# Optimization experiments

Hardware: AMD Instinct MI355X
Metric: run time of the kernel (lower is better)

The kernel has to match this reference:

```python
import jax, jax.numpy as jnp
import numpy as np

B, T, W, D = 2, 64, 32, 512
H = 8                      # n_heads
N = 64                     # d_state
EXPAND = 2
DIN = EXPAND * D           # 1024 d_inner
R = -(-D // 16)            # dt_rank = ceil(d_model/16) = 32
K = 4                      # d_conv (mamba default)


def setup_inputs():
    key = jax.random.key(0)
    ks = jax.random.split(key, 20)
    s = 0.02
    inp = {
        'x': jax.random.normal(ks[0], (B, T, W, D), jnp.float32),
        'wq': jax.random.normal(ks[1], (D, D), jnp.float32) * s,
        'bq': jnp.zeros((D,), jnp.float32),
        'wk': jax.random.normal(ks[2], (D, D), jnp.float32) * s,
        'bk': jnp.zeros((D,), jnp.float32),
        'wv': jax.random.normal(ks[3], (D, D), jnp.float32) * s,
        'bv': jnp.zeros((D,), jnp.float32),
        'wo': jax.random.normal(ks[4], (D, D), jnp.float32) * s,
        'bo': jnp.zeros((D,), jnp.float32),
        'in_proj_w': jax.random.normal(ks[5], (2 * DIN, D), jnp.float32) * s,
        'conv_w': jax.random.normal(ks[6], (DIN, 1, K), jnp.float32) * 0.2,
        'conv_b': jnp.zeros((DIN,), jnp.float32),
        'x_proj_w': jax.random.normal(ks[7], (R + 2 * N, DIN), jnp.float32) * s,
        'dt_proj_w': jax.random.normal(ks[8], (DIN, R), jnp.float32) * 0.1,
        'dt_proj_b': jnp.full((DIN,), -4.6, jnp.float32),  # ~softplus^-1(0.01)
        'A_log': jnp.log(jnp.broadcast_to(jnp.arange(1, N + 1, dtype=jnp.float32), (DIN, N))),
        'D_param': jnp.ones((DIN,), jnp.float32),
        'out_proj_w': jax.random.normal(ks[9], (D, DIN), jnp.float32) * s,
        'ln_w': jnp.ones((D,), jnp.float32),
        'ln_b': jnp.zeros((D,), jnp.float32),
    }
    return inp


def _attention(xf, wq, bq, wk, bk, wv, bv, wo, bo):
    b, L, d = xf.shape
    e = d // H
    q = (xf @ wq.T + bq).reshape(b, L, H, e)
    k = (xf @ wk.T + bk).reshape(b, L, H, e)
    v = (xf @ wv.T + bv).reshape(b, L, H, e)
    scale = 1.0 / jnp.sqrt(jnp.float32(e))
    scores = jnp.einsum('blhe,bshe->bhls', q, k) * scale
    causal = jnp.tril(jnp.ones((L, L), bool))
    scores = jnp.where(causal, scores, jnp.finfo(scores.dtype).min)
    attn = jax.nn.softmax(scores, axis=-1)  # dropout off (eval mode)
    out = jnp.einsum('bhls,bshe->blhe', attn, v).reshape(b, L, d)
    return out @ wo.T + bo


def _mamba(xf, in_proj_w, conv_w, conv_b, x_proj_w, dt_proj_w, dt_proj_b,
           A_log, D_param, out_proj_w):
    b, L, d = xf.shape
    xz = xf @ in_proj_w.T                 # (B,L,2*DIN)
    x_in, z = jnp.split(xz, 2, axis=-1)
    # causal depthwise conv1d over L
    xc = jnp.transpose(x_in, (0, 2, 1))   # (B,DIN,L)
    xc = jax.lax.conv_general_dilated(
        xc, conv_w, window_strides=(1,), padding=[(K - 1, 0)],
        feature_group_count=DIN, dimension_numbers=('NCH', 'OIH', 'NCH'))
    xc = xc + conv_b[None, :, None]
    u = jax.nn.silu(jnp.transpose(xc, (0, 2, 1)))   # (B,L,DIN)
    dbc = u @ x_proj_w.T                             # (B,L,R+2N)
    dt, Bm, Cm = dbc[..., :R], dbc[..., R:R + N], dbc[..., R + N:]
    dt = jax.nn.softplus(dt @ dt_proj_w.T + dt_proj_b)  # (B,L,DIN)
    A = -jnp.exp(A_log)                                 # (DIN,N)

    def step(h, t):
        dt_t, B_t, C_t, u_t = t  # (b,DIN),(b,N),(b,N),(b,DIN)
        dA = jnp.exp(dt_t[..., None] * A)                       # (b,DIN,N)
        h = dA * h + (dt_t * u_t)[..., None] * B_t[:, None, :]  # (b,DIN,N)
        y = jnp.einsum('bdn,bn->bd', h, C_t)
        return h, y

    h0 = jnp.zeros((b, DIN, N), xf.dtype)
    xs = (jnp.swapaxes(dt, 0, 1), jnp.swapaxes(Bm, 0, 1),
          jnp.swapaxes(Cm, 0, 1), jnp.swapaxes(u, 0, 1))
    _, ys = jax.lax.scan(step, h0, xs)
    y = jnp.swapaxes(ys, 0, 1) + u * D_param   # (B,L,DIN)
    y = y * jax.nn.silu(z)
    return y @ out_proj_w.T


def reference(x, wq, bq, wk, bk, wv, bv, wo, bo, in_proj_w, conv_w, conv_b,
              x_proj_w, dt_proj_w, dt_proj_b, A_log, D_param, out_proj_w,
              ln_w, ln_b):
    b, t, w, d = x.shape
    L = t * w
    xf = x.reshape(b, L, d)
    x_attn = _attention(xf, wq, bq, wk, bk, wv, bv, wo, bo).reshape(b, t, w, d)
    x_mamba = _mamba(xf, in_proj_w, conv_w, conv_b, x_proj_w, dt_proj_w,
                     dt_proj_b, A_log, D_param, out_proj_w).reshape(b, t, w, d)
    h = x + x_attn + x_mamba
    mu = jnp.mean(h, axis=-1, keepdims=True)
    var = jnp.mean(jnp.square(h - mu), axis=-1, keepdims=True)
    return (h - mu) * jax.lax.rsqrt(var + 1e-5) * ln_w + ln_b
```

## Files before the change

kernel.cpp:

```cpp
#include <hip/hip_runtime.h>

typedef __attribute__((ext_vector_type(4))) float f32x4;
typedef __attribute__((ext_vector_type(8))) short short8;
typedef __attribute__((ext_vector_type(2))) unsigned uint2e;

#define DEV static __device__ __forceinline__

DEV ushort f2b(float f) {
  union { float f; unsigned u; } v; v.f = f;
  unsigned r = v.u + 0x7FFF + ((v.u >> 16) & 1);
  return (ushort)(r >> 16);
}
DEV unsigned pack_bf2(float lo, float hi) {
  return (unsigned)f2b(lo) | ((unsigned)f2b(hi) << 16);
}
DEV float bflo(unsigned p) { return __uint_as_float(p << 16); }
DEV float bfhi(unsigned p) { return __uint_as_float(p & 0xFFFF0000u); }
DEV float b2f(ushort u) { return __uint_as_float((unsigned)u << 16); }

DEV float fexp2(float x) { float r; asm("v_exp_f32 %0, %1" : "=v"(r) : "v"(x)); return r; }

DEV float xor32_add_lo(float s) {
  uint2e r = __builtin_amdgcn_permlane32_swap(__float_as_uint(s), __float_as_uint(s), false, false);
  return s + __uint_as_float(r.x);
}

#define QP(x, ctrl) __int_as_float(__builtin_amdgcn_update_dpp(0, __float_as_int(x), (ctrl), 0xf, 0xf, false))
#define SWZ(x, off) __int_as_float(__builtin_amdgcn_ds_swizzle(__float_as_int(x), (off)))
#define DPP_ADD(x, ctrl, rmask) \
  ((x) + __int_as_float(__builtin_amdgcn_update_dpp(0, __float_as_int(x), (ctrl), (rmask), 0xf, false)))

#define LOG2E 1.44269504f

#define BB    2
#define LL    2048
#define DD    512
#define HH    8
#define EE    64
#define DIN   1024
#define NS    64
#define RR    32
#define BL    4096
#define NCH   16
#define TC    128
#define NC    1536
#define MFMA(a,b,c) __builtin_amdgcn_mfma_f32_16x16x32_bf16((a),(b),(c),0,0,0)

struct CvtJobs {
  const float* src[7];
  ushort*      dst[7];
  int          n[7];
};

__global__ __launch_bounds__(256) void cvt_multi(CvtJobs j) {
  int job = blockIdx.y;
  const float* s = j.src[job];
  ushort* d = j.dst[job];
  int n = j.n[job];
  for (int i = blockIdx.x * 256 + threadIdx.x; i < n; i += gridDim.x * 256)
    d[i] = f2b(s[i]);
}

__global__ __launch_bounds__(256) void pack_wcomb(
    const float* __restrict__ wo, const float* __restrict__ opw,
    const float* __restrict__ bq, const float* __restrict__ bk,
    const float* __restrict__ bv, ushort* __restrict__ wc,
    float* __restrict__ bqkv)
{
  int i = blockIdx.x * 256 + threadIdx.x;
  if (i < NC) bqkv[i] = (i < DD) ? bq[i] : ((i < 2 * DD) ? bk[i - DD] : bv[i - 2 * DD]);
  if (i >= DD * NC) return;
  int n = i / NC, c = i - n * NC;
  float v = (c < DD) ? wo[n * DD + c] : opw[n * DIN + (c - DD)];
  wc[i] = f2b(v);
}

__global__ __launch_bounds__(256) void gemm_bt(
    const ushort* __restrict__ A, const ushort* __restrict__ W,
    const float* __restrict__ bias, float* __restrict__ outF,
    ushort* __restrict__ outB, int M, int N, int K, int act)
{
  __shared__ ushort As[64][40];
  __shared__ ushort Ws[64][40];
  int m0 = blockIdx.y * 64, n0 = blockIdx.x * 64;
  int tid = threadIdx.x, l = tid & 63, w = tid >> 6;
  int wm = (w >> 1) * 32, wn = (w & 1) * 32;
  int lr = l & 15, kl = (l >> 4) * 8;
  int srow = tid >> 2, sk = (tid & 3) * 8;
  f32x4 acc[2][2] = {};

  for (int k0 = 0; k0 < K; k0 += 32) {
    uint4 av = *(const uint4*)&A[(size_t)(m0 + srow) * K + k0 + sk];
    uint4 wv;
    if (n0 + srow < N) wv = *(const uint4*)&W[(size_t)(n0 + srow) * K + k0 + sk];
    else { wv.x = 0; wv.y = 0; wv.z = 0; wv.w = 0; }
    *(uint4*)&As[srow][sk] = av;
    *(uint4*)&Ws[srow][sk] = wv;
    __syncthreads();
    short8 a0 = *(const short8*)&As[wm + lr][kl];
    short8 a1 = *(const short8*)&As[wm + 16 + lr][kl];
    short8 b0 = *(const short8*)&Ws[wn + lr][kl];
    short8 b1 = *(const short8*)&Ws[wn + 16 + lr][kl];
    acc[0][0] = MFMA(a0, b0, acc[0][0]);
    acc[0][1] = MFMA(a0, b1, acc[0][1]);
    acc[1][0] = MFMA(a1, b0, acc[1][0]);
    acc[1][1] = MFMA(a1, b1, acc[1][1]);
    __syncthreads();
  }

  #pragma unroll
  for (int mi = 0; mi < 2; mi++)
    #pragma unroll
    for (int ni = 0; ni < 2; ni++) {
      int rbase = m0 + wm + mi * 16 + ((l >> 4) << 2);
      int col = n0 + wn + ni * 16 + lr;
      if (col < N) {
        float bval = bias ? bias[col] : 0.f;
        #pragma unroll
        for (int r = 0; r < 4; r++) {
          float v = acc[mi][ni][r] + bval;
          if (act == 1) v = (v > 20.f) ? v : log1pf(__expf(v));
          size_t o = (size_t)(rbase + r) * N + col;
          if (outF) outF[o] = v;
          if (outB) outB[o] = f2b(v);
        }
      }
    }
}

__global__ __launch_bounds__(256) void gemm128(
    const ushort* __restrict__ A, const ushort* __restrict__ W,
    const float* __restrict__ bias, float* __restrict__ outF,
    ushort* __restrict__ outB, int M, int N, int K)
{
  __shared__ ushort As[128][40];
  __shared__ ushort Ws[128][40];
  int tid = threadIdx.x, l = tid & 63, w = tid >> 6;
  int m0 = blockIdx.y * 128, n0 = blockIdx.x * 128;
  int wm = (w >> 1) * 64, wn = (w & 1) * 64;
  int lr = l & 15, kl = (l >> 4) * 8;
  int srow = tid >> 1, sk = (tid & 1) * 16;
  f32x4 acc[4][4] = {};

  const ushort* Ap = A + (size_t)(m0 + srow) * K + sk;
  const ushort* Wp = W + (size_t)(n0 + srow) * K + sk;

  for (int k0 = 0; k0 < K; k0 += 32) {
    uint4 a0 = *(const uint4*)(Ap);
    uint4 a1 = *(const uint4*)(Ap + 8);
    uint4 b0 = *(const uint4*)(Wp);
    uint4 b1 = *(const uint4*)(Wp + 8);
    __syncthreads();
    *(uint4*)&As[srow][sk]     = a0;
    *(uint4*)&As[srow][sk + 8] = a1;
    *(uint4*)&Ws[srow][sk]     = b0;
    *(uint4*)&Ws[srow][sk + 8] = b1;
    __syncthreads();
    short8 af[4], bf[4];
    #pragma unroll
    for (int mi = 0; mi < 4; mi++) af[mi] = *(const short8*)&As[wm + mi * 16 + lr][kl];
    #pragma unroll
    for (int ni = 0; ni < 4; ni++) bf[ni] = *(const short8*)&Ws[wn + ni * 16 + lr][kl];
    #pragma unroll
    for (int mi = 0; mi < 4; mi++)
      #pragma unroll
      for (int ni = 0; ni < 4; ni++)
        acc[mi][ni] = MFMA(af[mi], bf[ni], acc[mi][ni]);
    Ap += 32; Wp += 32;
  }

  #pragma unroll
  for (int mi = 0; mi < 4; mi++)
    #pragma unroll
    for (int ni = 0; ni < 4; ni++) {
      int rbase = m0 + wm + mi * 16 + ((l >> 4) << 2);
      int col = n0 + wn + ni * 16 + lr;
      float bval = bias ? bias[col] : 0.f;
      #pragma unroll
      for (int r = 0; r < 4; r++) {
        float v = acc[mi][ni][r] + bval;
        size_t o = (size_t)(rbase + r) * N + col;
        if (outF) outF[o] = v;
        if (outB) outB[o] = f2b(v);
      }
    }
}

__global__ __launch_bounds__(256) void flash_attn(
    const ushort* __restrict__ qkv, ushort* __restrict__ comb)
{
  __shared__ ushort Qs[64][72];
  __shared__ ushort Ks[64][72];
  __shared__ ushort Vt[64][72];
  __shared__ ushort Ps[64][72];

  int qt = 31 - blockIdx.x;
  int h = blockIdx.y, b = blockIdx.z;
  int tid = threadIdx.x, l = tid & 63, w = tid >> 6;
  int w16 = w * 16, lr = l & 15, kl = (l >> 4) * 8;

  for (int i = tid; i < 512; i += 256) {
    int row = i >> 3, c8 = (i & 7) * 8;
    *(uint4*)&Qs[row][c8] =
        *(const uint4*)&qkv[((size_t)(b * LL + qt * 64 + row)) * NC + h * EE + c8];
  }
  __syncthreads();

  float m_r[4] = {-1e30f, -1e30f, -1e30f, -1e30f};
  float l_r[4] = {0.f, 0.f, 0.f, 0.f};
  f32x4 oacc[4] = {};
  const float SSC = 0.125f * LOG2E;

  for (int kv = 0; kv <= qt; kv++) {
    for (int i = tid; i < 512; i += 256) {
      int s = i >> 3, c8 = (i & 7) * 8;
      size_t rb = ((size_t)(b * LL + kv * 64 + s)) * NC + h * EE + c8;
      *(uint4*)&Ks[s][c8] = *(const uint4*)&qkv[rb + DD];
      uint4 vv = *(const uint4*)&qkv[rb + 2 * DD];
      const ushort* pv = (const ushort*)&vv;
      #pragma unroll
      for (int jj = 0; jj < 8; jj++) Vt[c8 + jj][s] = pv[jj];
    }
    __syncthreads();

    f32x4 sacc[4] = {};
    #pragma unroll
    for (int kk = 0; kk < 2; kk++) {
      short8 aq = *(const short8*)&Qs[w16 + lr][kk * 32 + kl];
      #pragma unroll
      for (int nt = 0; nt < 4; nt++) {
        short8 bk8 = *(const short8*)&Ks[nt * 16 + lr][kk * 32 + kl];
        sacc[nt] = MFMA(aq, bk8, sacc[nt]);
      }
    }

    bool diag = (kv == qt);
    float scl[4];
    #pragma unroll
    for (int r = 0; r < 4; r++) {
      int rloc = w16 + ((l >> 4) << 2) + r;
      float sv[4];
      #pragma unroll
      for (int nt = 0; nt < 4; nt++) {
        float v = sacc[nt][r] * SSC;
        if (diag && (nt * 16 + lr) > rloc) v = -1e30f;
        sv[nt] = v;
      }
      float mx = fmaxf(fmaxf(sv[0], sv[1]), fmaxf(sv[2], sv[3]));
      mx = fmaxf(mx, QP(mx, 0xB1));
      mx = fmaxf(mx, QP(mx, 0x4E));
      mx = fmaxf(mx, SWZ(mx, 0x101F));
      mx = fmaxf(mx, SWZ(mx, 0x201F));
      float mnew = fmaxf(m_r[r], mx);
      float sc = fexp2(m_r[r] - mnew);
      float rs = 0.f;
      #pragma unroll
      for (int nt = 0; nt < 4; nt++) {
        float p = fexp2(sv[nt] - mnew);
        rs += p;
        Ps[rloc][nt * 16 + lr] = f2b(p);
      }
      rs += QP(rs, 0xB1);
      rs += QP(rs, 0x4E);
      rs += SWZ(rs, 0x101F);
      rs += SWZ(rs, 0x201F);
      l_r[r] = l_r[r] * sc + rs;
      m_r[r] = mnew;
      scl[r] = sc;
    }
    #pragma unroll
    for (int nt = 0; nt < 4; nt++)
      #pragma unroll
      for (int r = 0; r < 4; r++) oacc[nt][r] *= scl[r];

    #pragma unroll
    for (int kk = 0; kk < 2; kk++) {
      short8 ap = *(const short8*)&Ps[w16 + lr][kk * 32 + kl];
      #pragma unroll
      for (int nt = 0; nt < 4; nt++) {
        short8 bv8 = *(const short8*)&Vt[nt * 16 + lr][kk * 32 + kl];
        oacc[nt] = MFMA(ap, bv8, oacc[nt]);
      }
    }
    __syncthreads();
  }

  #pragma unroll
  for (int nt = 0; nt < 4; nt++)
    #pragma unroll
    for (int r = 0; r < 4; r++) {
      int row = qt * 64 + w16 + ((l >> 4) << 2) + r;
      float v = oacc[nt][r] / l_r[r];
      comb[((size_t)(b * LL + row)) * NC + h * EE + nt * 16 + lr] = f2b(v);
    }
}

__global__ __launch_bounds__(256) void conv_silu(
    const ushort* __restrict__ xz, const float* __restrict__ cw,
    const float* __restrict__ cb, ushort* __restrict__ ub)
{
  int i = blockIdx.x * 256 + threadIdx.x;
  if (i >= BL * DIN) return;
  int d = i & (DIN - 1);
  int bl = i >> 10;
  int t = bl & (LL - 1);
  int b = bl >> 11;
  float s = cb[d];
  #pragma unroll
  for (int j = 0; j < 4; j++) {
    int tt = t - 3 + j;
    if (tt >= 0) s += b2f(xz[((size_t)(b * LL + tt)) * (2 * DIN) + d]) * cw[d * 4 + j];
  }
  float r = s / (1.f + __expf(-s));
  ub[i] = f2b(r);
}

__global__ __launch_bounds__(256) void slice_dt(
    const float* __restrict__ dbc, ushort* __restrict__ dtc)
{
  int i = blockIdx.x * 256 + threadIdx.x;
  if (i >= BL * RR) return;
  int m = i >> 5, r = i & 31;
  dtc[i] = f2b(dbc[m * 160 + r]);
}

__global__ __launch_bounds__(256) void pack_bc(
    const float* __restrict__ dbc, unsigned* __restrict__ bbp,
    float4* __restrict__ bcp4)
{
  int i = blockIdx.x * 256 + threadIdx.x;
  if (i >= BB * (LL / 2) * NS) return;
  int n = i & 63, tp = (i >> 6) & 1023, b = i >> 16;
  size_t r0 = ((size_t)(b * LL + 2 * tp)) * 160;
  float B0 = dbc[r0 + 32 + n],  C0 = dbc[r0 + 96 + n];
  float B1 = dbc[r0 + 192 + n], C1 = dbc[r0 + 256 + n];
  bbp[i] = pack_bf2(B0, B1);
  bcp4[i] = make_float4(B0, C0, B1, C1);
}

__global__ __launch_bounds__(256) void pack_dtu(
    const ushort* __restrict__ dtb16, const ushort* __restrict__ ub,
    const ushort* __restrict__ xz, const float* __restrict__ dpar,
    unsigned* __restrict__ dtu_p, unsigned* __restrict__ sg_p)
{
  __shared__ float s_dt[32][65], s_du[32][65], s_gz[32][65], s_ug[32][65];
  int d0 = blockIdx.x * 64, t0 = blockIdx.y * 32;
  int tid = threadIdx.x;
  int c = tid & 63, r4 = tid >> 6;
  float Dv = dpar[d0 + c];
  #pragma unroll
  for (int k = 0; k < 8; k++) {
    int r = k * 4 + r4;
    size_t row = (size_t)(t0 + r);
    float dtv = b2f(dtb16[row * DIN + d0 + c]);
    float uv  = b2f(ub   [row * DIN + d0 + c]);
    float zz  = b2f(xz   [row * (2 * DIN) + DIN + d0 + c]);
    float g = zz / (1.f + __expf(-zz));
    s_dt[r][c] = dtv;
    s_du[r][c] = dtv * uv;
    s_gz[r][c] = g;
    s_ug[r][c] = uv * Dv * g;
  }
  __syncthreads();
  int dl = tid >> 2, q = tid & 3;
  int b = t0 >> 11, tl0 = t0 & (LL - 1);
  size_t obase = ((size_t)(b * DIN + d0 + dl)) * LL + tl0 + q * 8;
  #pragma unroll
  for (int tt = 0; tt < 8; tt++) {
    int t = q * 8 + tt;
    dtu_p[obase + tt] = pack_bf2(s_dt[t][dl], s_du[t][dl]);
    sg_p [obase + tt] = pack_bf2(s_gz[t][dl], s_ug[t][dl]);
  }
}

__global__ __launch_bounds__(256) void scan_phase1(
    const unsigned* __restrict__ dtu_p, const unsigned* __restrict__ bbp,
    const float* __restrict__ alog, float* __restrict__ hf, float* __restrict__ ap)
{
  __shared__ float lds[4][TC][2];
  int tid = threadIdx.x, w = tid >> 6, l = tid & 63;
  int wid = blockIdx.x * 4 + w;
  int d = wid & (DIN - 1);
  int c = (wid >> 10) & (NCH - 1);
  int b = wid >> 14;
  float An2 = -__expf(alog[d * NS + l]) * LOG2E;

  size_t pbase = ((size_t)(b * DIN + d)) * LL + c * TC;
  unsigned p0 = dtu_p[pbase + l];
  unsigned p1 = dtu_p[pbase + 64 + l];
  float s0 = bflo(p0), s1 = bflo(p1);
  s0 = DPP_ADD(s0, 0x111, 0xf); s0 = DPP_ADD(s0, 0x112, 0xf);
  s0 = DPP_ADD(s0, 0x114, 0xf); s0 = DPP_ADD(s0, 0x118, 0xf);
  s0 = DPP_ADD(s0, 0x142, 0xa); s0 = DPP_ADD(s0, 0x143, 0xc);
  s1 = DPP_ADD(s1, 0x111, 0xf); s1 = DPP_ADD(s1, 0x112, 0xf);
  s1 = DPP_ADD(s1, 0x114, 0xf); s1 = DPP_ADD(s1, 0x118, 0xf);
  s1 = DPP_ADD(s1, 0x142, 0xa); s1 = DPP_ADD(s1, 0x143, 0xc);
  float T0 = __uint_as_float(__builtin_amdgcn_readlane(__float_as_uint(s0), 63));
  float T  = T0 + __uint_as_float(__builtin_amdgcn_readlane(__float_as_uint(s1), 63));
  lds[w][l][0]      = T - s0;
  lds[w][l][1]      = bfhi(p0);
  lds[w][64 + l][0] = (T - T0) - s1;
  lds[w][64 + l][1] = bfhi(p1);
  __syncthreads();

  const unsigned* bq = bbp + ((size_t)(b * 1024 + c * 64) * 64 + l);
  float h0 = 0.f, h1 = 0.f;
  for (int g = 0; g < 16; g++) {
    unsigned bv[4];
    #pragma unroll
    for (int k = 0; k < 4; k++) bv[k] = bq[k * 64];
    const float* gb = &lds[w][g * 8][0];
    #pragma unroll
    for (int j = 0; j < 8; j++) {
      float2 dd = *(const float2*)(gb + j * 2);
      float Bv = (j & 1) ? bfhi(bv[j >> 1]) : bflo(bv[j >> 1]);
      float a = fexp2(dd.x * An2);
      if (j & 1) h1 += a * (dd.y * Bv);
      else       h0 += a * (dd.y * Bv);
    }
    bq += 256;
  }
  size_t o = (((size_t)((b << 10) + d) * NCH) + c) * 64 + l;
  hf[o] = h0 + h1;
  ap[o] = fexp2(T * An2);
}

__global__ __launch_bounds__(256) void scan_carry(
    const float* __restrict__ hf, const float* __restrict__ ap,
    float* __restrict__ carry)
{
  int i = blockIdx.x * 256 + threadIdx.x;
  int n = i & 63;
  int d = (i >> 6) & (DIN - 1);
  int b = i >> 16;
  size_t base = ((size_t)((b << 10) + d) * NCH) * 64 + n;
  float cur = 0.f;
  #pragma unroll
  for (int c = 0; c < NCH; c++) {
    carry[base + (size_t)c * 64] = cur;
    cur = ap[base + (size_t)c * 64] * cur + hf[base + (size_t)c * 64];
  }
}

__global__ __launch_bounds__(256) void scan_phase3(
    const unsigned* __restrict__ dtu_p, const unsigned* __restrict__ sg_p,
    const float4* __restrict__ bcp4, const float* __restrict__ alog,
    const float* __restrict__ carry, ushort* __restrict__ ymt)
{
  __shared__ float lds[4][TC][4];
  __shared__ ushort yt[4][TC];
  int tid = threadIdx.x, w = tid >> 6, l = tid & 63;
  int wid = blockIdx.x * 4 + w;
  int d = wid & (DIN - 1);
  int c = (wid >> 10) & (NCH - 1);
  int b = wid >> 14;
  float An2 = -__expf(alog[d * NS + l]) * LOG2E;

  size_t pbase = ((size_t)(b * DIN + d)) * LL + c * TC;
  #pragma unroll
  for (int q = 0; q < 2; q++) {
    unsigned pd = dtu_p[pbase + q * 64 + l];
    unsigned pg = sg_p [pbase + q * 64 + l];
    lds[w][q * 64 + l][0] = bflo(pd);
    lds[w][q * 64 + l][1] = bfhi(pd);
    lds[w][q * 64 + l][2] = bflo(pg);
    lds[w][q * 64 + l][3] = bfhi(pg);
  }
  __syncthreads();

  float h = carry[(((size_t)((b << 10) + d) * NCH) + c) * 64 + l];
  const float4* bq = bcp4 + ((size_t)(b * 1024 + c * 64) * 64 + l);
  bool s1f = l & 1, s2f = l & 2, s4f = l & 4;
  bool wl = l < 8;

  for (int g = 0; g < 16; g++) {
    float4 bcs[4];
    bcs[0] = bq[0]; bcs[1] = bq[64]; bcs[2] = bq[128]; bcs[3] = bq[192];
    const float* gb = &lds[w][g * 8][0];
    float p[8];
    #pragma unroll
    for (int j = 0; j < 8; j++) {
      float2 dd = *(const float2*)(gb + j * 4);
      float Bv = (j & 1) ? bcs[j >> 1].z : bcs[j >> 1].x;
      float Cv = (j & 1) ? bcs[j >> 1].w : bcs[j >> 1].y;
      float a = fexp2(dd.x * An2);
      h = a * h + dd.y * Bv;
      p[j] = h * Cv;
    }
    #pragma unroll
    for (int j = 0; j < 8; j++) p[j] += QP(p[j], 0xB1);
    float q0 = s1f ? p[1] : p[0];
    float q1 = s1f ? p[3] : p[2];
    float q2 = s1f ? p[5] : p[4];
    float q3 = s1f ? p[7] : p[6];
    q0 += QP(q0, 0x4E); q1 += QP(q1, 0x4E);
    q2 += QP(q2, 0x4E); q3 += QP(q3, 0x4E);
    float r0 = s2f ? q1 : q0;
    float r1 = s2f ? q3 : q2;
    r0 += SWZ(r0, 0x101F); r1 += SWZ(r1, 0x101F);
    float s = s4f ? r1 : r0;
    s += QP(s, 0x128);
    s += SWZ(s, 0x401F);
    s = xor32_add_lo(s);

    float2 sgv = *(const float2*)(&lds[w][g * 8 + (l & 7)][2]);
    if (wl) yt[w][g * 8 + l] = f2b(s * sgv.x + sgv.y);
    bq += 256;
  }
  __syncthreads();
  unsigned vv = *(const unsigned*)&yt[w][2 * l];
  ((unsigned*)(ymt + pbase))[l] = vv;
}

__global__ __launch_bounds__(256) void transpose_ym(
    const ushort* __restrict__ ymt, ushort* __restrict__ comb)
{
  __shared__ ushort tile[64][72];
  int tid = threadIdx.x;
  int bx = blockIdx.x;
  int by = blockIdx.y;
  int b  = blockIdx.z;
  int r = tid >> 2, c16 = (tid & 3) * 16;
  const ushort* src = ymt + ((size_t)(b * DIN + bx * 64 + r)) * LL + by * 64 + c16;
  *(uint4*)&tile[r][c16]     = *(const uint4*)src;
  *(uint4*)&tile[r][c16 + 8] = *(const uint4*)(src + 8);
  __syncthreads();
  ushort tmp[16];
  #pragma unroll
  for (int j = 0; j < 16; j++) tmp[j] = tile[c16 + j][r];
  ushort* dst = comb + ((size_t)(b * LL + by * 64 + r)) * NC + DD + bx * 64 + c16;
  *(uint4*)dst       = *(uint4*)&tmp[0];
  *(uint4*)(dst + 8) = *(uint4*)&tmp[8];
}

__global__ __launch_bounds__(256) void residual_ln(
    const float* __restrict__ x, const float* __restrict__ so,
    const float* __restrict__ lw, const float* __restrict__ lb,
    float* __restrict__ out)
{
  int row = blockIdx.x * 4 + (threadIdx.x >> 6);
  int l = threadIdx.x & 63;
  size_t base = (size_t)row * DD;
  float h[8];
  float s = 0.f, s2 = 0.f;
  #pragma unroll
  for (int half = 0; half < 2; half++) {
    int c = half * 256 + l * 4;
    float4 xv = *(const float4*)(x + base + c);
    float4 sv = *(const float4*)(so + base + c);
    float* hp = h + half * 4;
    hp[0] = xv.x + sv.x;
    hp[1] = xv.y + sv.y;
    hp[2] = xv.z + sv.z;
    hp[3] = xv.w + sv.w;
    #pragma unroll
    for (int j = 0; j < 4; j++) { s += hp[j]; s2 += hp[j] * hp[j]; }
  }
  #pragma unroll
  for (int o = 1; o < 64; o <<= 1) { s += __shfl_xor(s, o); s2 += __shfl_xor(s2, o); }
  float mean = s * (1.f / DD);
  float var = s2 * (1.f / DD) - mean * mean;
  float rs = rsqrtf(var + 1e-5f);
  #pragma unroll
  for (int half = 0; half < 2; half++) {
    int c = half * 256 + l * 4;
    float4 ov;
    ov.x = (h[half*4+0] - mean) * rs * lw[c+0] + lb[c+0];
    ov.y = (h[half*4+1] - mean) * rs * lw[c+1] + lb[c+1];
    ov.z = (h[half*4+2] - mean) * rs * lw[c+2] + lb[c+2];
    ov.w = (h[half*4+3] - mean) * rs * lw[c+3] + lb[c+3];
    *(float4*)(out + base + c) = ov;
  }
}

extern "C" void kernel_launch(void* const* d_in, const int* in_sizes, int n_in,
                              void* d_out, int out_size, void* d_ws, size_t ws_size,
                              hipStream_t stream) {
  const float* x    = (const float*)d_in[0];
  const float* wq   = (const float*)d_in[1];
  const float* bq   = (const float*)d_in[2];
  const float* wk   = (const float*)d_in[3];
  const float* bk   = (const float*)d_in[4];
  const float* wv   = (const float*)d_in[5];
  const float* bv   = (const float*)d_in[6];
  const float* wo   = (const float*)d_in[7];
  const float* bo   = (const float*)d_in[8];
  const float* inw  = (const float*)d_in[9];
  const float* cw   = (const float*)d_in[10];
  const float* cb   = (const float*)d_in[11];
  const float* xpw  = (const float*)d_in[12];
  const float* dtw  = (const float*)d_in[13];
  const float* dtb  = (const float*)d_in[14];
  const float* alog = (const float*)d_in[15];
  const float* dpar = (const float*)d_in[16];
  const float* opw  = (const float*)d_in[17];
  const float* lnw  = (const float*)d_in[18];
  const float* lnb  = (const float*)d_in[19];

  char* ws = (char*)d_ws;
  size_t off = 0;
  auto alloc = [&](size_t bytes) -> void* {
    void* p = ws + off;
    off += (bytes + 255) & ~(size_t)255;
    return p;
  };

  const size_t BLD = (size_t)BL * DD;
  const size_t BLDIN = (size_t)BL * DIN;
  const size_t BLNC = (size_t)BL * NC;

  ushort* xf_b   = (ushort*)alloc(BLD * 2);
  ushort* wqkv_b = (ushort*)alloc((size_t)NC * DD * 2);
  float*  bqkv   = (float*)alloc(NC * 4);
  ushort* inw_b  = (ushort*)alloc(2 * DIN * DD * 2);
  ushort* xpw_b  = (ushort*)alloc(160 * DIN * 2);
  ushort* dtw_b  = (ushort*)alloc(DIN * RR * 2);
  ushort* wcomb_b= (ushort*)alloc((size_t)DD * NC * 2);
  ushort* qkv_b  = (ushort*)alloc(BLNC * 2);
  ushort* comb_a = (ushort*)alloc(BLNC * 2);
  float*  sum_o  = (float*)alloc(BLD * 4);
  ushort* xz_b   = (ushort*)alloc(BL * (size_t)(2 * DIN) * 2);
  ushort* u_b    = (ushort*)alloc(BLDIN * 2);
  float*  dbc    = (float*)alloc((size_t)BL * 160 * 4);
  ushort* dtc_b  = (ushort*)alloc((size_t)BL * RR * 2);
  ushort* dt_b   = (ushort*)alloc(BLDIN * 2);
  ushort* ymt_b  = (ushort*)alloc(BLDIN * 2);
  unsigned* bbp  = (unsigned*)alloc((size_t)BB * (LL / 2) * NS * 4);
  float4* bcp4   = (float4*)alloc((size_t)BB * (LL / 2) * NS * sizeof(float4));
  unsigned* dtu_p = (unsigned*)alloc(BLDIN * 4);
  unsigned* sg_p  = (unsigned*)alloc(BLDIN * 4);

  const size_t SCN = (size_t)BB * DIN * NCH * 64;
  float* hf_s    = (float*)xz_b;
  float* ap_s    = hf_s + SCN;
  float* carry_s = (float*)alloc(SCN * 4);

  CvtJobs cj;
  cj.src[0] = x;    cj.dst[0] = xf_b;                 cj.n[0] = (int)BLD;
  cj.src[1] = wq;   cj.dst[1] = wqkv_b;               cj.n[1] = DD * DD;
  cj.src[2] = wk;   cj.dst[2] = wqkv_b + DD * DD;     cj.n[2] = DD * DD;
  cj.src[3] = wv;   cj.dst[3] = wqkv_b + 2 * DD * DD; cj.n[3] = DD * DD;
  cj.src[4] = inw;  cj.dst[4] = inw_b;                cj.n[4] = 2 * DIN * DD;
  cj.src[5] = xpw;  cj.dst[5] = xpw_b;                cj.n[5] = 160 * DIN;
  cj.src[6] = dtw;  cj.dst[6] = dtw_b;                cj.n[6] = DIN * RR;
  cvt_multi<<<dim3(256, 7), 256, 0, stream>>>(cj);
  pack_wcomb<<<dim3((DD * NC + 255) / 256), 256, 0, stream>>>(wo, opw, bq, bk, bv, wcomb_b, bqkv);

  gemm128<<<dim3(12, 32), 256, 0, stream>>>(xf_b, wqkv_b, bqkv, nullptr, qkv_b, BL, NC, DD);

  flash_attn<<<dim3(32, HH, BB), 256, 0, stream>>>(qkv_b, comb_a);

  gemm128<<<dim3(16, 32), 256, 0, stream>>>(xf_b, inw_b, nullptr, nullptr, xz_b, BL, 2 * DIN, DD);

  conv_silu<<<dim3(32768), 256, 0, stream>>>(xz_b, cw, cb, u_b);

  gemm_bt<<<dim3(3, 64), 256, 0, stream>>>(u_b, xpw_b, nullptr, dbc, nullptr, BL, 160, DIN, 0);

  slice_dt<<<dim3(512), 256, 0, stream>>>(dbc, dtc_b);
  gemm_bt<<<dim3(16, 64), 256, 0, stream>>>(dtc_b, dtw_b, dtb, nullptr, dt_b, BL, DIN, RR, 1);

  pack_bc<<<dim3(512), 256, 0, stream>>>(dbc, bbp, bcp4);
  pack_dtu<<<dim3(16, 128), 256, 0, stream>>>(dt_b, u_b, xz_b, dpar, dtu_p, sg_p);
  scan_phase1<<<dim3(8192), 256, 0, stream>>>(dtu_p, bbp, alog, hf_s, ap_s);
  scan_carry<<<dim3(512), 256, 0, stream>>>(hf_s, ap_s, carry_s);
  scan_phase3<<<dim3(8192), 256, 0, stream>>>(dtu_p, sg_p, bcp4, alog, carry_s, ymt_b);
  transpose_ym<<<dim3(16, 32, BB), 256, 0, stream>>>(ymt_b, comb_a);

  gemm_bt<<<dim3(8, 64), 256, 0, stream>>>(comb_a, wcomb_b, bo, sum_o, nullptr, BL, DD, NC, 0);

  residual_ln<<<dim3(1024), 256, 0, stream>>>(x, sum_o, lnw, lnb, (float*)d_out);
}
```

Baseline: 398.5 us.

## Merge QKV and in_proj GEMMs and co-schedule attention with x_proj GEMM

Concatenates the QKV and Mamba in_proj weights into a single 3584-wide GEMM, so one launch produces q, k, v, x and z in a shared buffer. The flash attention kernel and the x_proj GEMM are then merged into one launch whose first 512 blocks do attention and whose remaining blocks do the small x_proj GEMM. The aim is to cut launch count and let the small GEMM fill idle CUs left by the causally imbalanced attention tail. The cost is a wider row stride for the attention and conv reads, and a simpler 64x64 x_proj tile path.

Result: faster. 380.1 us (-4.6%).

```diff
diff --git a/kernel.cpp b/kernel.cpp
--- a/kernel.cpp
+++ b/kernel.cpp
@@ -44,6 +44,9 @@
 #define NCH   16
 #define TC    128
 #define NC    1536
+#define NQ    3584
+#define XOFF  1536
+#define ZOFF  2560
 #define MFMA(a,b,c) __builtin_amdgcn_mfma_f32_16x16x32_bf16((a),(b),(c),0,0,0)
 
 struct CvtJobs {
@@ -65,10 +68,11 @@
     const float* __restrict__ wo, const float* __restrict__ opw,
     const float* __restrict__ bq, const float* __restrict__ bk,
     const float* __restrict__ bv, ushort* __restrict__ wc,
-    float* __restrict__ bqkv)
+    float* __restrict__ bqi)
 {
   int i = blockIdx.x * 256 + threadIdx.x;
-  if (i < NC) bqkv[i] = (i < DD) ? bq[i] : ((i < 2 * DD) ? bk[i - DD] : bv[i - 2 * DD]);
+  if (i < NQ)
+    bqi[i] = (i < DD) ? bq[i] : (i < 2 * DD) ? bk[i - DD] : (i < NC) ? bv[i - 2 * DD] : 0.f;
   if (i >= DD * NC) return;
   int n = i / NC, c = i - n * NC;
   float v = (c < DD) ? wo[n * DD + c] : opw[n * DIN + (c - DD)];
@@ -186,113 +190,161 @@
     }
 }
 
-__global__ __launch_bounds__(256) void flash_attn(
-    const ushort* __restrict__ qkv, ushort* __restrict__ comb)
-{
-  __shared__ ushort Qs[64][72];
-  __shared__ ushort Ks[64][72];
-  __shared__ ushort Vt[64][72];
-  __shared__ ushort Ps[64][72];
-
-  int qt = 31 - blockIdx.x;
-  int h = blockIdx.y, b = blockIdx.z;
+__global__ __launch_bounds__(256) void attn_xproj(
+    const ushort* __restrict__ qkv, ushort* __restrict__ comb,
+    const ushort* __restrict__ ub, const ushort* __restrict__ xpw,
+    float* __restrict__ dbc)
+{
+  __shared__ ushort smem[4 * 64 * 72];
+  int id = blockIdx.x;
   int tid = threadIdx.x, l = tid & 63, w = tid >> 6;
-  int w16 = w * 16, lr = l & 15, kl = (l >> 4) * 8;
-
-  for (int i = tid; i < 512; i += 256) {
-    int row = i >> 3, c8 = (i & 7) * 8;
-    *(uint4*)&Qs[row][c8] =
-        *(const uint4*)&qkv[((size_t)(b * LL + qt * 64 + row)) * NC + h * EE + c8];
-  }
-  __syncthreads();
-
-  float m_r[4] = {-1e30f, -1e30f, -1e30f, -1e30f};
-  float l_r[4] = {0.f, 0.f, 0.f, 0.f};
-  f32x4 oacc[4] = {};
-  const float SSC = 0.125f * LOG2E;
-
-  for (int kv = 0; kv <= qt; kv++) {
+
+  if (id < 512) {
+    typedef ushort row72[72];
+    row72* Qs = (row72*)smem;
+    row72* Ks = Qs + 64;
+    row72* Vt = Ks + 64;
+    row72* Ps = Vt + 64;
+    int qt = 31 - (id & 31), h = (id >> 5) & 7, b = id >> 8;
+    int w16 = w * 16, lr = l & 15, kl = (l >> 4) * 8;
+
     for (int i = tid; i < 512; i += 256) {
-      int s = i >> 3, c8 = (i & 7) * 8;
-      size_t rb = ((size_t)(b * LL + kv * 64 + s)) * NC + h * EE + c8;
-      *(uint4*)&Ks[s][c8] = *(const uint4*)&qkv[rb + DD];
-      uint4 vv = *(const uint4*)&qkv[rb + 2 * DD];
-      const ushort* pv = (const ushort*)&vv;
-      #pragma unroll
-      for (int jj = 0; jj < 8; jj++) Vt[c8 + jj][s] = pv[jj];
+      int row = i >> 3, c8 = (i & 7) * 8;
+      *(uint4*)&Qs[row][c8] =
+          *(const uint4*)&qkv[((size_t)(b * LL + qt * 64 + row)) * NQ + h * EE + c8];
     }
     __syncthreads();
 
-    f32x4 sacc[4] = {};
-    #pragma unroll
-    for (int kk = 0; kk < 2; kk++) {
-      short8 aq = *(const short8*)&Qs[w16 + lr][kk * 32 + kl];
+    float m_r[4] = {-1e30f, -1e30f, -1e30f, -1e30f};
+    float l_r[4] = {0.f, 0.f, 0.f, 0.f};
+    f32x4 oacc[4] = {};
+    const float SSC = 0.125f * LOG2E;
+
+    for (int kv = 0; kv <= qt; kv++) {
+      for (int i = tid; i < 512; i += 256) {
+        int s = i >> 3, c8 = (i & 7) * 8;
+        size_t rb = ((size_t)(b * LL + kv * 64 + s)) * NQ + h * EE + c8;
+        *(uint4*)&Ks[s][c8] = *(const uint4*)&qkv[rb + DD];
+        uint4 vv = *(const uint4*)&qkv[rb + 2 * DD];
+        const ushort* pv = (const ushort*)&vv;
+        #pragma unroll
+        for (int jj = 0; jj < 8; jj++) Vt[c8 + jj][s] = pv[jj];
+      }
+      __syncthreads();
+
+      f32x4 sacc[4] = {};
       #pragma unroll
-      for (int nt = 0; nt < 4; nt++) {
-        short8 bk8 = *(const short8*)&Ks[nt * 16 + lr][kk * 32 + kl];
-        sacc[nt] = MFMA(aq, bk8, sacc[nt]);
+      for (int kk = 0; kk < 2; kk++) {
+        short8 aq = *(const short8*)&Qs[w16 + lr][kk * 32 + kl];
+        #pragma unroll
+        for (int nt = 0; nt < 4; nt++) {
+          short8 bk8 = *(const short8*)&Ks[nt * 16 + lr][kk * 32 + kl];
+          sacc[nt] = MFMA(aq, bk8, sacc[nt]);
+        }
       }
+
+      bool diag = (kv == qt);
+      float scl[4];
+      #pragma unroll
+      for (int r = 0; r < 4; r++) {
+        int rloc = w16 + ((l >> 4) << 2) + r;
+        float sv[4];
+        #pragma unroll
+        for (int nt = 0; nt < 4; nt++) {
+          float v = sacc[nt][r] * SSC;
+          if (diag && (nt * 16 + lr) > rloc) v = -1e30f;
+          sv[nt] = v;
+        }
+        float mx = fmaxf(fmaxf(sv[0], sv[1]), fmaxf(sv[2], sv[3]));
+        mx = fmaxf(mx, QP(mx, 0xB1));
+        mx = fmaxf(mx, QP(mx, 0x4E));
+        mx = fmaxf(mx, SWZ(mx, 0x101F));
+        mx = fmaxf(mx, SWZ(mx, 0x201F));
+        float mnew = fmaxf(m_r[r], mx);
+        float sc = fexp2(m_r[r] - mnew);
+        float rs = 0.f;
+        #pragma unroll
+        for (int nt = 0; nt < 4; nt++) {
+          float p = fexp2(sv[nt] - mnew);
+          rs += p;
+          Ps[rloc][nt * 16 + lr] = f2b(p);
+        }
+        rs += QP(rs, 0xB1);
+        rs += QP(rs, 0x4E);
+        rs += SWZ(rs, 0x101F);
+        rs += SWZ(rs, 0x201F);
+        l_r[r] = l_r[r] * sc + rs;
+        m_r[r] = mnew;
+        scl[r] = sc;
+      }
+      #pragma unroll
+      for (int nt = 0; nt < 4; nt++)
+        #pragma unroll
+        for (int r = 0; r < 4; r++) oacc[nt][r] *= scl[r];
+
+      #pragma unroll
+      for (int kk = 0; kk < 2; kk++) {
+        short8 ap = *(const short8*)&Ps[w16 + lr][kk * 32 + kl];
+        #pragma unroll
+        for (int nt = 0; nt < 4; nt++) {
+          short8 bv8 = *(const short8*)&Vt[nt * 16 + lr][kk * 32 + kl];
+          oacc[nt] = MFMA(ap, bv8, oacc[nt]);
+        }
+      }
+      __syncthreads();
     }
 
-    bool diag = (kv == qt);
-    float scl[4];
-    #pragma unroll
-    for (int r = 0; r < 4; r++) {
-      int rloc = w16 + ((l >> 4) << 2) + r;
-      float sv[4];
-      #pragma unroll
-      for (int nt = 0; nt < 4; nt++) {
-        float v = sacc[nt][r] * SSC;
-        if (diag && (nt * 16 + lr) > rloc) v = -1e30f;
-        sv[nt] = v;
-      }
-      float mx = fmaxf(fmaxf(sv[0], sv[1]), fmaxf(sv[2], sv[3]));
-      mx = fmaxf(mx, QP(mx, 0xB1));
-      mx = fmaxf(mx, QP(mx, 0x4E));
-      mx = fmaxf(mx, SWZ(mx, 0x101F));
-      mx = fmaxf(mx, SWZ(mx, 0x201F));
-      float mnew = fmaxf(m_r[r], mx);
-      float sc = fexp2(m_r[r] - mnew);
-      float rs = 0.f;
-      #pragma unroll
-      for (int nt = 0; nt < 4; nt++) {
-        float p = fexp2(sv[nt] - mnew);
-        rs += p;
-        Ps[rloc][nt * 16 + lr] = f2b(p);
-      }
-      rs += QP(rs, 0xB1);
-      rs += QP(rs, 0x4E);
-      rs += SWZ(rs, 0x101F);
-      rs += SWZ(rs, 0x201F);
-      l_r[r] = l_r[r] * sc + rs;
-      m_r[r] = mnew;
-      scl[r] = sc;
-    }
     #pragma unroll
     for (int nt = 0; nt < 4; nt++)
       #pragma unroll
-      for (int r = 0; r < 4; r++) oacc[nt][r] *= scl[r];
-
-    #pragma unroll
-    for (int kk = 0; kk < 2; kk++) {
-      short8 ap = *(const short8*)&Ps[w16 + lr][kk * 32 + kl];
+      for (int r = 0; r < 4; r++) {
+        int row = qt * 64 + w16 + ((l >> 4) << 2) + r;
+        float v = oacc[nt][r] / l_r[r];
+        comb[((size_t)(b * LL + row)) * NC + h * EE + nt * 16 + lr] = f2b(v);
+      }
+  } else {
+    typedef ushort row40[40];
+    row40* As = (row40*)smem;
+    row40* Ws = As + 64;
+    int rid = id - 512;
+    int n0 = (rid % 3) * 64, m0 = (rid / 3) * 64;
+    int wm = (w >> 1) * 32, wn = (w & 1) * 32;
+    int lr = l & 15, kl = (l >> 4) * 8;
+    int srow = tid >> 2, sk = (tid & 3) * 8;
+    f32x4 acc[2][2] = {};
+
+    for (int k0 = 0; k0 < DIN; k0 += 32) {
+      uint4 av = *(const uint4*)&ub[(size_t)(m0 + srow) * DIN + k0 + sk];
+      uint4 wv;
+      if (n0 + srow < 160) wv = *(const uint4*)&xpw[(size_t)(n0 + srow) * DIN + k0 + sk];
+      else { wv.x = 0; wv.y = 0; wv.z = 0; wv.w = 0; }
+      *(uint4*)&As[srow][sk] = av;
+      *(uint4*)&Ws[srow][sk] = wv;
+      __syncthreads();
+      short8 a0 = *(const short8*)&As[wm + lr][kl];
+      short8 a1 = *(const short8*)&As[wm + 16 + lr][kl];
+      short8 b0 = *(const short8*)&Ws[wn + lr][kl];
+      short8 b1 = *(const short8*)&Ws[wn + 16 + lr][kl];
+      acc[0][0] = MFMA(a0, b0, acc[0][0]);
+      acc[0][1] = MFMA(a0, b1, acc[0][1]);
+      acc[1][0] = MFMA(a1, b0, acc[1][0]);
+      acc[1][1] = MFMA(a1, b1, acc[1][1]);
+      __syncthreads();
+    }
+
+    #pragma unroll
+    for (int mi = 0; mi < 2; mi++)
       #pragma unroll
-      for (int nt = 0; nt < 4; nt++) {
-        short8 bv8 = *(const short8*)&Vt[nt * 16 + lr][kk * 32 + kl];
-        oacc[nt] = MFMA(ap, bv8, oacc[nt]);
+      for (int ni = 0; ni < 2; ni++) {
+        int rbase = m0 + wm + mi * 16 + ((l >> 4) << 2);
+        int col = n0 + wn + ni * 16 + lr;
+        if (col < 160) {
+          #pragma unroll
+          for (int r = 0; r < 4; r++)
+            dbc[(size_t)(rbase + r) * 160 + col] = acc[mi][ni][r];
+        }
       }
-    }
-    __syncthreads();
-  }
-
-  #pragma unroll
-  for (int nt = 0; nt < 4; nt++)
-    #pragma unroll
-    for (int r = 0; r < 4; r++) {
-      int row = qt * 64 + w16 + ((l >> 4) << 2) + r;
-      float v = oacc[nt][r] / l_r[r];
-      comb[((size_t)(b * LL + row)) * NC + h * EE + nt * 16 + lr] = f2b(v);
-    }
+  }
 }
 
 __global__ __launch_bounds__(256) void conv_silu(
@@ -309,7 +361,7 @@
   #pragma unroll
   for (int j = 0; j < 4; j++) {
     int tt = t - 3 + j;
-    if (tt >= 0) s += b2f(xz[((size_t)(b * LL + tt)) * (2 * DIN) + d]) * cw[d * 4 + j];
+    if (tt >= 0) s += b2f(xz[((size_t)(b * LL + tt)) * NQ + XOFF + d]) * cw[d * 4 + j];
   }
   float r = s / (1.f + __expf(-s));
   ub[i] = f2b(r);
@@ -354,7 +406,7 @@
     size_t row = (size_t)(t0 + r);
     float dtv = b2f(dtb16[row * DIN + d0 + c]);
     float uv  = b2f(ub   [row * DIN + d0 + c]);
-    float zz  = b2f(xz   [row * (2 * DIN) + DIN + d0 + c]);
+    float zz  = b2f(xz   [row * NQ + ZOFF + d0 + c]);
     float g = zz / (1.f + __expf(-zz));
     s_dt[r][c] = dtv;
     s_du[r][c] = dtv * uv;
@@ -607,19 +659,16 @@
 
   const size_t BLD = (size_t)BL * DD;
   const size_t BLDIN = (size_t)BL * DIN;
-  const size_t BLNC = (size_t)BL * NC;
 
   ushort* xf_b   = (ushort*)alloc(BLD * 2);
-  ushort* wqkv_b = (ushort*)alloc((size_t)NC * DD * 2);
-  float*  bqkv   = (float*)alloc(NC * 4);
-  ushort* inw_b  = (ushort*)alloc(2 * DIN * DD * 2);
+  ushort* wqi_b  = (ushort*)alloc((size_t)NQ * DD * 2);
+  float*  bqi    = (float*)alloc(NQ * 4);
   ushort* xpw_b  = (ushort*)alloc(160 * DIN * 2);
   ushort* dtw_b  = (ushort*)alloc(DIN * RR * 2);
   ushort* wcomb_b= (ushort*)alloc((size_t)DD * NC * 2);
-  ushort* qkv_b  = (ushort*)alloc(BLNC * 2);
-  ushort* comb_a = (ushort*)alloc(BLNC * 2);
+  ushort* qkvxz_b= (ushort*)alloc((size_t)BL * NQ * 2);
+  ushort* comb_a = (ushort*)alloc((size_t)BL * NC * 2);
   float*  sum_o  = (float*)alloc(BLD * 4);
-  ushort* xz_b   = (ushort*)alloc(BL * (size_t)(2 * DIN) * 2);
   ushort* u_b    = (ushort*)alloc(BLDIN * 2);
   float*  dbc    = (float*)alloc((size_t)BL * 160 * 4);
   ushort* dtc_b  = (ushort*)alloc((size_t)BL * RR * 2);
@@ -631,36 +680,32 @@
   unsigned* sg_p  = (unsigned*)alloc(BLDIN * 4);
 
   const size_t SCN = (size_t)BB * DIN * NCH * 64;
-  float* hf_s    = (float*)xz_b;
+  float* hf_s    = (float*)qkvxz_b;
   float* ap_s    = hf_s + SCN;
   float* carry_s = (float*)alloc(SCN * 4);
 
   CvtJobs cj;
-  cj.src[0] = x;    cj.dst[0] = xf_b;                 cj.n[0] = (int)BLD;
-  cj.src[1] = wq;   cj.dst[1] = wqkv_b;               cj.n[1] = DD * DD;
-  cj.src[2] = wk;   cj.dst[2] = wqkv_b + DD * DD;     cj.n[2] = DD * DD;
-  cj.src[3] = wv;   cj.dst[3] = wqkv_b + 2 * DD * DD; cj.n[3] = DD * DD;
-  cj.src[4] = inw;  cj.dst[4] = inw_b;                cj.n[4] = 2 * DIN * DD;
-  cj.src[5] = xpw;  cj.dst[5] = xpw_b;                cj.n[5] = 160 * DIN;
-  cj.src[6] = dtw;  cj.dst[6] = dtw_b;                cj.n[6] = DIN * RR;
+  cj.src[0] = x;    cj.dst[0] = xf_b;                cj.n[0] = (int)BLD;
+  cj.src[1] = wq;   cj.dst[1] = wqi_b;               cj.n[1] = DD * DD;
+  cj.src[2] = wk;   cj.dst[2] = wqi_b + DD * DD;     cj.n[2] = DD * DD;
+  cj.src[3] = wv;   cj.dst[3] = wqi_b + 2 * DD * DD; cj.n[3] = DD * DD;
+  cj.src[4] = inw;  cj.dst[4] = wqi_b + 3 * DD * DD; cj.n[4] = 2 * DIN * DD;
+  cj.src[5] = xpw;  cj.dst[5] = xpw_b;               cj.n[5] = 160 * DIN;
+  cj.src[6] = dtw;  cj.dst[6] = dtw_b;               cj.n[6] = DIN * RR;
   cvt_multi<<<dim3(256, 7), 256, 0, stream>>>(cj);
-  pack_wcomb<<<dim3((DD * NC + 255) / 256), 256, 0, stream>>>(wo, opw, bq, bk, bv, wcomb_b, bqkv);
-
-  gemm128<<<dim3(12, 32), 256, 0, stream>>>(xf_b, wqkv_b, bqkv, nullptr, qkv_b, BL, NC, DD);
-
-  flash_attn<<<dim3(32, HH, BB), 256, 0, stream>>>(qkv_b, comb_a);
-
-  gemm128<<<dim3(16, 32), 256, 0, stream>>>(xf_b, inw_b, nullptr, nullptr, xz_b, BL, 2 * DIN, DD);
-
-  conv_silu<<<dim3(32768), 256, 0, stream>>>(xz_b, cw, cb, u_b);
-
-  gemm_bt<<<dim3(3, 64), 256, 0, stream>>>(u_b, xpw_b, nullptr, dbc, nullptr, BL, 160, DIN, 0);
+  pack_wcomb<<<dim3((DD * NC + 255) / 256), 256, 0, stream>>>(wo, opw, bq, bk, bv, wcomb_b, bqi);
+
+  gemm128<<<dim3(28, 32), 256, 0, stream>>>(xf_b, wqi_b, bqi, nullptr, qkvxz_b, BL, NQ, DD);
+
+  conv_silu<<<dim3(32768), 256, 0, stream>>>(qkvxz_b, cw, cb, u_b);
+
+  attn_xproj<<<dim3(704), 256, 0, stream>>>(qkvxz_b, comb_a, u_b, xpw_b, dbc);
 
   slice_dt<<<dim3(512), 256, 0, stream>>>(dbc, dtc_b);
   gemm_bt<<<dim3(16, 64), 256, 0, stream>>>(dtc_b, dtw_b, dtb, nullptr, dt_b, BL, DIN, RR, 1);
 
   pack_bc<<<dim3(512), 256, 0, stream>>>(dbc, bbp, bcp4);
-  pack_dtu<<<dim3(16, 128), 256, 0, stream>>>(dt_b, u_b, xz_b, dpar, dtu_p, sg_p);
+  pack_dtu<<<dim3(16, 128), 256, 0, stream>>>(dt_b, u_b, qkvxz_b, dpar, dtu_p, sg_p);
   scan_phase1<<<dim3(8192), 256, 0, stream>>>(dtu_p, bbp, alog, hf_s, ap_s);
   scan_carry<<<dim3(512), 256, 0, stream>>>(hf_s, ap_s, carry_s);
   scan_phase3<<<dim3(8192), 256, 0, stream>>>(dtu_p, sg_p, bcp4, alog, carry_s, ymt_b);
```
